# Kernel tuning notes

Hardware: AMD Instinct MI355X
Metric: run time of the kernel (lower is better)

The kernel has to match this reference:

```python
import jax, jax.numpy as jnp
import numpy as np

B, A, D, H = 32, 64, 128, 512
F = A * D  # 8192

def setup_inputs() -> dict:
    key = jax.random.key(0)
    ks = jax.random.split(key, 20)
    s = 0.02
    return {
        "swarm_states": jax.random.normal(ks[0], (B, A, D), jnp.float32),
        "swarm_goals": jax.random.normal(ks[1], (B, A, D), jnp.float32),
        # quantum layer stand-in: Linear(F->F) + tanh
        "Wq": jax.random.normal(ks[2], (F, F), jnp.float32) * s,
        "bq": jnp.zeros((F,), jnp.float32),
        # interaction_net: Linear(2D->H) ReLU Linear(H->H) ReLU Linear(H->D)
        "Wi1": jax.random.normal(ks[3], (2 * D, H), jnp.float32) * s,
        "bi1": jnp.zeros((H,), jnp.float32),
        "Wi2": jax.random.normal(ks[4], (H, H), jnp.float32) * s,
        "bi2": jnp.zeros((H,), jnp.float32),
        "Wi3": jax.random.normal(ks[5], (H, D), jnp.float32) * s,
        "bi3": jnp.zeros((D,), jnp.float32),
        # coordination_net: Linear(F->H) ReLU Linear(H->H) ReLU Linear(H->F)
        "Wc1": jax.random.normal(ks[6], (F, H), jnp.float32) * s,
        "bc1": jnp.zeros((H,), jnp.float32),
        "Wc2": jax.random.normal(ks[7], (H, H), jnp.float32) * s,
        "bc2": jnp.zeros((H,), jnp.float32),
        "Wc3": jax.random.normal(ks[8], (H, F), jnp.float32) * s,
        "bc3": jnp.zeros((F,), jnp.float32),
    }

def reference(swarm_states, swarm_goals, Wq, bq, Wi1, bi1, Wi2, bi2, Wi3, bi3,
              Wc1, bc1, Wc2, bc2, Wc3, bc3):
    b, a, d = swarm_states.shape
    states_flat = swarm_states.reshape(b, a * d)
    # quantum feature extraction (stand-in for QuantumNeuralLayer)
    quantum_features = jnp.tanh(states_flat @ Wq + bq)  # (B, A*D)

    # vectorized pairwise interaction MLP over all ordered (i, j) pairs
    xi = jnp.broadcast_to(swarm_states[:, :, None, :], (b, a, a, d))
    xj = jnp.broadcast_to(swarm_states[:, None, :, :], (b, a, a, d))
    pair = jnp.concatenate([xi, xj], axis=-1)            # (B, A, A, 2D)
    h = jax.nn.relu(pair @ Wi1 + bi1)
    h = jax.nn.relu(h @ Wi2 + bi2)
    inter = h @ Wi3 + bi3                                # (B, A, A, D)
    offdiag = (1.0 - jnp.eye(a, dtype=inter.dtype))[None, :, :, None]
    # per-agent aggregation over the other agents (mean over j != i)
    interactions = (inter * offdiag).sum(axis=2) / (a - 1)  # (B, A, D)

    c = jax.nn.relu(quantum_features @ Wc1 + bc1)
    c = jax.nn.relu(c @ Wc2 + bc2)
    coordination = (c @ Wc3 + bc3).reshape(b, a, d)      # (B, A, D)

    coordinated_states = swarm_states + 0.1 * interactions + 0.1 * coordination
    return coordinated_states, quantum_features, interactions, coordination
```

## Files before the change

kernel.cpp:

```cpp
#include <hip/hip_runtime.h>

typedef __attribute__((ext_vector_type(8))) short bf16x8;
typedef __attribute__((ext_vector_type(16))) float f32x16;
typedef _Float16 f16;
typedef __attribute__((ext_vector_type(8))) _Float16 f16x8;

static __device__ __forceinline__ unsigned short f2bf(float x) {
  unsigned int u = __float_as_uint(x);
  return (unsigned short)((u + 0x7FFFu + ((u >> 16) & 1u)) >> 16);
}
static __device__ __forceinline__ unsigned int pk2bf(float lo, float hi) {
  return ((unsigned int)f2bf(hi) << 16) | f2bf(lo);
}

static __device__ __forceinline__ f16x8 relu8(f16x8 x) {
  f16x8 z = {0, 0, 0, 0, 0, 0, 0, 0};
  return __builtin_elementwise_max(x, z);
}

__global__ __launch_bounds__(256) void tobf_kernel(const float* __restrict__ src,
                                                   unsigned short* __restrict__ dst) {
  const int idx = blockIdx.x * 256 + threadIdx.x;
  float4 v = ((const float4*)src)[idx];
  ushort4 o;
  o.x = f2bf(v.x); o.y = f2bf(v.y); o.z = f2bf(v.z); o.w = f2bf(v.w);
  ((ushort4*)dst)[idx] = o;
}

__global__ __launch_bounds__(256) void w2h_kernel(const float* __restrict__ Wi2,
                                                  f16* __restrict__ W2h) {
  __shared__ float tile[32][33];
  const int t = threadIdx.x;
  const int bk = blockIdx.x, bn = blockIdx.y;
  const int r = t >> 5, c = t & 31;
#pragma unroll
  for (int p = 0; p < 4; p++) {
    int rr = p * 8 + r;
    tile[rr][c] = Wi2[(bk * 32 + rr) * 512 + bn * 32 + c];
  }
  __syncthreads();
#pragma unroll
  for (int p = 0; p < 4; p++) {
    int rr = p * 8 + r;
    W2h[(bn * 32 + rr) * 512 + bk * 32 + c] = (f16)tile[c][rr];
  }
}

__global__ __launch_bounds__(256) void uvh_kernel(const float* __restrict__ S,
                                                  const float* __restrict__ Wi1,
                                                  const float* __restrict__ bi1,
                                                  f16* __restrict__ Uh, f16* __restrict__ Vh) {
  __shared__ float st[128][12];
  const int t = threadIdx.x;
  const int row0 = blockIdx.x * 8;
  for (int idx = t; idx < 1024; idx += 256) {
    int r = idx >> 7, k = idx & 127;
    st[k][r] = S[(row0 + r) * 128 + k];
  }
  __syncthreads();
  float au0[8], au1[8], av0[8], av1[8];
#pragma unroll
  for (int r = 0; r < 8; r++) { au0[r] = 0.f; au1[r] = 0.f; av0[r] = 0.f; av1[r] = 0.f; }
#pragma unroll 4
  for (int k = 0; k < 128; k++) {
    float wt0 = Wi1[k * 512 + t];
    float wt1 = Wi1[k * 512 + 256 + t];
    float wb0 = Wi1[(k + 128) * 512 + t];
    float wb1 = Wi1[(k + 128) * 512 + 256 + t];
    float4 sA = *(const float4*)&st[k][0];
    float4 sB = *(const float4*)&st[k][4];
    float s8[8] = {sA.x, sA.y, sA.z, sA.w, sB.x, sB.y, sB.z, sB.w};
#pragma unroll
    for (int r = 0; r < 8; r++) {
      au0[r] += s8[r] * wt0;
      au1[r] += s8[r] * wt1;
      av0[r] += s8[r] * wb0;
      av1[r] += s8[r] * wb1;
    }
  }
  const float b0 = bi1[t], b1 = bi1[256 + t];
#pragma unroll
  for (int r = 0; r < 8; r++) {
    Uh[(row0 + r) * 512 + t]       = (f16)(au0[r] + b0);
    Uh[(row0 + r) * 512 + 256 + t] = (f16)(au1[r] + b1);
    Vh[(row0 + r) * 512 + t]       = (f16)av0[r];
    Vh[(row0 + r) * 512 + 256 + t] = (f16)av1[r];
  }
}

__global__ __launch_bounds__(256, 4) void gemmw(const unsigned short* __restrict__ Abf,
                                                const float* __restrict__ W,
                                                float* __restrict__ P,
                                                int K, int N, int L, int l4sh) {
  __shared__ __align__(16) unsigned short As[32 * 512];
  const int t = threadIdx.x;
  const int k0 = blockIdx.y * L;
  const int L4 = L >> 2;
  const int swzm = 2 * L - 1;
  for (int idx = t; idx < (L << 3); idx += 256) {
    int row = idx >> l4sh, k4 = idx & (L4 - 1);
    ushort4 a4 = *(const ushort4*)&Abf[(size_t)row * K + k0 + k4 * 4];
    int off = (row * 2 * L + k4 * 8) ^ (((row & 7) << 4) & swzm);
    *(ushort4*)((char*)As + off) = a4;
  }
  __syncthreads();
  const int lane = t & 63, w = t >> 6;
  const int lrow = lane & 31, lh = lane >> 5;
  const int col = blockIdx.x * 128 + w * 32 + lrow;
  f32x16 acc0, acc1;
#pragma unroll
  for (int r = 0; r < 16; r++) { acc0[r] = 0.f; acc1[r] = 0.f; }
  const float* Wp = W + (size_t)(k0 + lh * 8) * N + col;
  const int aswz = ((lrow & 7) << 4) & swzm;
  const int abase = lrow * 2 * L + lh * 16;
  const int nks = L >> 4;
  int ks = 0;
  for (; ks + 1 < nks; ks += 2) {
    float wv0[8], wv1[8];
#pragma unroll
    for (int jj = 0; jj < 8; jj++) wv0[jj] = Wp[(size_t)(ks * 16 + jj) * N];
#pragma unroll
    for (int jj = 0; jj < 8; jj++) wv1[jj] = Wp[(size_t)(ks * 16 + 16 + jj) * N];
    uint4 b0, b1;
    b0.x = pk2bf(wv0[0], wv0[1]); b0.y = pk2bf(wv0[2], wv0[3]);
    b0.z = pk2bf(wv0[4], wv0[5]); b0.w = pk2bf(wv0[6], wv0[7]);
    b1.x = pk2bf(wv1[0], wv1[1]); b1.y = pk2bf(wv1[2], wv1[3]);
    b1.z = pk2bf(wv1[4], wv1[5]); b1.w = pk2bf(wv1[6], wv1[7]);
    bf16x8 af0 = *(const bf16x8*)((const char*)As + ((abase + ks * 32) ^ aswz));
    bf16x8 af1 = *(const bf16x8*)((const char*)As + ((abase + ks * 32 + 32) ^ aswz));
    acc0 = __builtin_amdgcn_mfma_f32_32x32x16_bf16(af0, *(const bf16x8*)&b0, acc0, 0, 0, 0);
    acc1 = __builtin_amdgcn_mfma_f32_32x32x16_bf16(af1, *(const bf16x8*)&b1, acc1, 0, 0, 0);
  }
  if (ks < nks) {
    float wv0[8];
#pragma unroll
    for (int jj = 0; jj < 8; jj++) wv0[jj] = Wp[(size_t)(ks * 16 + jj) * N];
    uint4 b0;
    b0.x = pk2bf(wv0[0], wv0[1]); b0.y = pk2bf(wv0[2], wv0[3]);
    b0.z = pk2bf(wv0[4], wv0[5]); b0.w = pk2bf(wv0[6], wv0[7]);
    bf16x8 af0 = *(const bf16x8*)((const char*)As + ((abase + ks * 32) ^ aswz));
    acc0 = __builtin_amdgcn_mfma_f32_32x32x16_bf16(af0, *(const bf16x8*)&b0, acc0, 0, 0, 0);
  }
  float* Pr = P + (size_t)blockIdx.y * 32 * N + col;
#pragma unroll
  for (int r = 0; r < 16; r++) {
    int row = (r & 3) + 8 * (r >> 2) + 4 * lh;
    Pr[(size_t)row * N] = acc0[r] + acc1[r];
  }
}

__global__ __launch_bounds__(256) void reduce_kernel(const float* __restrict__ P,
                                                     const float* __restrict__ bias,
                                                     float* __restrict__ dst,
                                                     unsigned short* __restrict__ dstbf,
                                                     int lnN, int KS, int act, int wbf) {
  const int idx = blockIdx.x * 256 + threadIdx.x;
  const int N = 1 << lnN;
  const int m = idx >> lnN, n = idx & (N - 1);
  float s = 0.f;
#pragma unroll 8
  for (int p = 0; p < KS; p++) s += P[((size_t)(p * 32 + m) << lnN) + n];
  s += bias[n];
  if (act == 1) s = fmaxf(s, 0.f);
  else if (act == 2) s = tanhf(s);
  dst[idx] = s;
  if (wbf) dstbf[idx] = f2bf(s);
}

__global__ __launch_bounds__(512, 2) void inter6_kernel(const f16* __restrict__ Uh,
                                                        const f16* __restrict__ Vh,
                                                        const f16* __restrict__ W2h,
                                                        const float* __restrict__ bi2,
                                                        float* __restrict__ Hsum) {
  __shared__ __align__(16) f16 Bt[128 * 512];
  __shared__ __align__(16) f16 Vc[64 * 128];
  const int t = threadIdx.x;
  const int nq = blockIdx.x;

#pragma unroll
  for (int i = 0; i < 16; i++) {
    int idx = i * 512 + t;
    int n = idx >> 6, ch = idx & 63;
    f16x8 w8 = *(const f16x8*)&W2h[(size_t)(nq * 128 + n) * 512 + ch * 8];
    int off = (n * 1024 + ch * 16) ^ ((n & 15) << 4);
    *(f16x8*)((char*)Bt + off) = w8;
  }

  const int w = t >> 6, lane = t & 63;
  const int ii = w & 1, tg = w >> 1;
  const int lrow = lane & 31, lh = lane >> 5;
  const char* Btc = (const char*)Bt;
  const char* Vcc = (const char*)Vc;
  char* Vcw = (char*)Vc;

  int bofs[4], bswz[4];
#pragma unroll
  for (int nf = 0; nf < 4; nf++) {
    int nr = nf * 32 + lrow;
    bofs[nf] = nr * 1024 + lh * 16;
    bswz[nf] = (nr & 15) << 4;
  }
  const int vofs0 = lrow * 256;
  const int vswz0 = (lrow & 15) << 4;
  const int vofs1 = (lrow + 32) * 256;
  const int vswz1 = vswz0;

  const int b = blockIdx.y >> 1;

  for (int s = 0; s < 4; s++) {
    const int tid = blockIdx.y * 16 + tg * 4 + s;
    const int it = tid & 31;
    const f16* Ub = Uh + (size_t)(b * 64 + it * 2 + ii) * 512 + lh * 8;

    f32x16 acc[2][4];
#pragma unroll
    for (int mf = 0; mf < 2; mf++)
#pragma unroll
      for (int nf = 0; nf < 4; nf++)
#pragma unroll
        for (int r = 0; r < 16; r++) acc[mf][nf][r] = 0.f;

    for (int ch = 0; ch < 4; ch++) {
      const int kc = ch * 128;
      __syncthreads();
#pragma unroll
      for (int i = 0; i < 2; i++) {
        int idx = i * 512 + t;
        int row = idx >> 4, c8 = idx & 15;
        f16x8 w8 = *(const f16x8*)&Vh[(size_t)(b * 64 + row) * 512 + kc + c8 * 8];
        *(f16x8*)(Vcw + ((row * 256 + c8 * 16) ^ ((row & 15) << 4))) = w8;
      }
      __syncthreads();
#pragma unroll
      for (int k16 = 0; k16 < 8; k16++) {
        const int kb2 = k16 * 32 + lh * 16;
        f16x8 v0 = *(const f16x8*)(Vcc + ((vofs0 + kb2) ^ vswz0));
        f16x8 v1 = *(const f16x8*)(Vcc + ((vofs1 + kb2) ^ vswz1));
        f16x8 u0 = *(const f16x8*)(Ub + kc + k16 * 16);
        f16x8 a0 = relu8(v0 + u0);
        f16x8 a1 = relu8(v1 + u0);
        const int kbyte = (kc + k16 * 16) * 2 + lh * 16 - lh * 16;
        (void)kbyte;
#pragma unroll
        for (int nf = 0; nf < 4; nf++) {
          f16x8 bfr = *(const f16x8*)(Btc + ((bofs[nf] + (kc + k16 * 16) * 2) ^ bswz[nf]));
          acc[0][nf] = __builtin_amdgcn_mfma_f32_32x32x16_f16(a0, bfr, acc[0][nf], 0, 0, 0);
          acc[1][nf] = __builtin_amdgcn_mfma_f32_32x32x16_f16(a1, bfr, acc[1][nf], 0, 0, 0);
        }
      }
    }

    const int iglob = it * 2 + ii;
    const int mf_d = iglob >> 5;
    const int rd = iglob & 31;
    const int lh_d = (rd >> 2) & 1;
    const int r_d = (rd & 3) + 4 * (rd >> 3);
#pragma unroll
    for (int nf = 0; nf < 4; nf++) {
      const int col = nq * 128 + nf * 32 + lrow;
      const float b2 = bi2[col];
      float ssum = 0.f;
#pragma unroll
      for (int mf = 0; mf < 2; mf++)
#pragma unroll
        for (int r = 0; r < 16; r++) {
          float x = fmaxf(acc[mf][nf][r] + b2, 0.f);
          if (mf == mf_d && r == r_d && lh == lh_d) x = 0.f;
          ssum += x;
        }
      ssum += __shfl_xor(ssum, 32);
      if (lh == 0) Hsum[(size_t)(b * 64 + iglob) * 512 + col] = ssum;
    }
  }
}

__global__ __launch_bounds__(256) void k3_kernel(const float* __restrict__ Hsum,
                                                 const float* __restrict__ Wi3,
                                                 const float* __restrict__ bi3,
                                                 float* __restrict__ inter) {
  __shared__ float st[512][10];
  const int t = threadIdx.x;
  const int row0 = blockIdx.x * 8;
  for (int idx = t; idx < 4096; idx += 256) {
    int r = idx >> 9, k = idx & 511;
    st[k][r] = Hsum[(row0 + r) * 512 + k] * (1.0f / 63.0f);
  }
  __syncthreads();
  const int c = t & 63;
  const int rg = t >> 6;
  float a0[2] = {0.f, 0.f}, a1[2] = {0.f, 0.f};
#pragma unroll 4
  for (int k = 0; k < 512; k++) {
    float w0 = Wi3[k * 128 + c];
    float w1 = Wi3[k * 128 + 64 + c];
    float2 h = *(const float2*)&st[k][rg * 2];
    a0[0] += h.x * w0; a0[1] += h.y * w0;
    a1[0] += h.x * w1; a1[1] += h.y * w1;
  }
  float b0 = bi3[c], b1 = bi3[64 + c];
#pragma unroll
  for (int r = 0; r < 2; r++) {
    inter[(row0 + rg * 2 + r) * 128 + c]      = a0[r] + b0;
    inter[(row0 + rg * 2 + r) * 128 + 64 + c] = a1[r] + b1;
  }
}

__global__ __launch_bounds__(256) void combine_kernel(const float* __restrict__ S,
                                                      const float* __restrict__ inter,
                                                      const float* __restrict__ coord,
                                                      float* __restrict__ out0) {
  const int i = blockIdx.x * 256 + threadIdx.x;
  float4 s = ((const float4*)S)[i];
  float4 a = ((const float4*)inter)[i];
  float4 c = ((const float4*)coord)[i];
  float4 o;
  o.x = s.x + 0.1f * (a.x + c.x);
  o.y = s.y + 0.1f * (a.y + c.y);
  o.z = s.z + 0.1f * (a.z + c.z);
  o.w = s.w + 0.1f * (a.w + c.w);
  ((float4*)out0)[i] = o;
}

extern "C" void kernel_launch(void* const* d_in, const int* in_sizes, int n_in,
                              void* d_out, int out_size, void* d_ws, size_t ws_size,
                              hipStream_t stream) {
  const float* states = (const float*)d_in[0];
  const float* Wq  = (const float*)d_in[2];
  const float* bq  = (const float*)d_in[3];
  const float* Wi1 = (const float*)d_in[4];
  const float* bi1 = (const float*)d_in[5];
  const float* Wi2 = (const float*)d_in[6];
  const float* bi2 = (const float*)d_in[7];
  const float* Wi3 = (const float*)d_in[8];
  const float* bi3 = (const float*)d_in[9];
  const float* Wc1 = (const float*)d_in[10];
  const float* bc1 = (const float*)d_in[11];
  const float* Wc2 = (const float*)d_in[12];
  const float* bc2 = (const float*)d_in[13];
  const float* Wc3 = (const float*)d_in[14];
  const float* bc3 = (const float*)d_in[15];

  float* out   = (float*)d_out;
  float* out0  = out;
  float* qf    = out + 262144;
  float* inter = out + 524288;
  float* coord = out + 786432;

  char* ws = (char*)d_ws;
  float*          P    = (float*)(ws);
  f16*            Uh   = (f16*)(ws + ((size_t)16 << 20));
  f16*            Vh   = (f16*)(ws + ((size_t)19 << 20));
  f16*            W2h  = (f16*)(ws + ((size_t)22 << 20));
  float*          Hsum = (float*)(ws + ((size_t)23 << 20));
  unsigned short* Sbf  = (unsigned short*)(ws + ((size_t)27 << 20));
  unsigned short* qfbf = (unsigned short*)(ws + ((size_t)28 << 20));
  float*          c1   = (float*)(ws + ((size_t)29 << 20));
  float*          c2   = (float*)(ws + ((size_t)29 << 20) + (1 << 16));
  unsigned short* c1bf = (unsigned short*)(ws + ((size_t)29 << 20) + (2 << 16));
  unsigned short* c2bf = (unsigned short*)(ws + ((size_t)29 << 20) + (3 << 16));

  tobf_kernel<<<256, 256, 0, stream>>>(states, Sbf);
  w2h_kernel<<<dim3(16, 16), 256, 0, stream>>>(Wi2, W2h);
  uvh_kernel<<<256, 256, 0, stream>>>(states, Wi1, bi1, Uh, Vh);

  gemmw<<<dim3(64, 16), 256, 0, stream>>>(Sbf, Wq, P, 8192, 8192, 512, 7);
  reduce_kernel<<<1024, 256, 0, stream>>>(P, bq, qf, qfbf, 13, 16, 2, 1);

  inter6_kernel<<<dim3(4, 64), 512, 0, stream>>>(Uh, Vh, W2h, bi2, Hsum);
  k3_kernel<<<256, 256, 0, stream>>>(Hsum, Wi3, bi3, inter);

  gemmw<<<dim3(4, 64), 256, 0, stream>>>(qfbf, Wc1, P, 8192, 512, 128, 5);
  reduce_kernel<<<64, 256, 0, stream>>>(P, bc1, c1, c1bf, 9, 64, 1, 1);
  gemmw<<<dim3(4, 32), 256, 0, stream>>>(c1bf, Wc2, P, 512, 512, 16, 2);
  reduce_kernel<<<64, 256, 0, stream>>>(P, bc2, c2, c2bf, 9, 32, 1, 1);
  gemmw<<<dim3(64, 8), 256, 0, stream>>>(c2bf, Wc3, P, 512, 8192, 64, 4);
  reduce_kernel<<<1024, 256, 0, stream>>>(P, bc3, coord, qfbf, 13, 8, 0, 0);

  combine_kernel<<<256, 256, 0, stream>>>(states, inter, coord, out0);
}
```

Before: 225.6 us.

## Merge prep and tail kernels, co-schedule k3 with Wc1 GEMM, prefetch weights

Three prep kernels are merged into one block-indexed prep kernel. The k3 projection and the Wc1 split-K GEMM are fused into one launch so their blocks run concurrently. The final combine is folded into the last reduce. The gemmw inner loop now software-prefetches four weight fragments ahead of the MFMAs, clamped at the K edge, to hide global-load latency. This cuts launch count and exposes overlap, at the cost of more registers and a larger shared allocation for the fused kernel.

```diff
diff --git a/kernel.cpp b/kernel.cpp
--- a/kernel.cpp
+++ b/kernel.cpp
@@ -12,89 +12,101 @@
 static __device__ __forceinline__ unsigned int pk2bf(float lo, float hi) {
   return ((unsigned int)f2bf(hi) << 16) | f2bf(lo);
 }
-
 static __device__ __forceinline__ f16x8 relu8(f16x8 x) {
   f16x8 z = {0, 0, 0, 0, 0, 0, 0, 0};
   return __builtin_elementwise_max(x, z);
 }
 
-__global__ __launch_bounds__(256) void tobf_kernel(const float* __restrict__ src,
-                                                   unsigned short* __restrict__ dst) {
-  const int idx = blockIdx.x * 256 + threadIdx.x;
-  float4 v = ((const float4*)src)[idx];
-  ushort4 o;
-  o.x = f2bf(v.x); o.y = f2bf(v.y); o.z = f2bf(v.z); o.w = f2bf(v.w);
-  ((ushort4*)dst)[idx] = o;
-}
-
-__global__ __launch_bounds__(256) void w2h_kernel(const float* __restrict__ Wi2,
-                                                  f16* __restrict__ W2h) {
-  __shared__ float tile[32][33];
+__global__ __launch_bounds__(256) void prep_kernel(const float* __restrict__ states,
+                                                   const float* __restrict__ Wi2,
+                                                   const float* __restrict__ Wi1,
+                                                   const float* __restrict__ bi1,
+                                                   unsigned short* __restrict__ Sbf,
+                                                   f16* __restrict__ W2h,
+                                                   f16* __restrict__ Uh, f16* __restrict__ Vh) {
+  __shared__ float lds_f[1536];
   const int t = threadIdx.x;
-  const int bk = blockIdx.x, bn = blockIdx.y;
-  const int r = t >> 5, c = t & 31;
-#pragma unroll
-  for (int p = 0; p < 4; p++) {
-    int rr = p * 8 + r;
-    tile[rr][c] = Wi2[(bk * 32 + rr) * 512 + bn * 32 + c];
-  }
-  __syncthreads();
-#pragma unroll
-  for (int p = 0; p < 4; p++) {
-    int rr = p * 8 + r;
-    W2h[(bn * 32 + rr) * 512 + bk * 32 + c] = (f16)tile[c][rr];
-  }
-}
-
-__global__ __launch_bounds__(256) void uvh_kernel(const float* __restrict__ S,
-                                                  const float* __restrict__ Wi1,
-                                                  const float* __restrict__ bi1,
-                                                  f16* __restrict__ Uh, f16* __restrict__ Vh) {
-  __shared__ float st[128][12];
-  const int t = threadIdx.x;
-  const int row0 = blockIdx.x * 8;
-  for (int idx = t; idx < 1024; idx += 256) {
-    int r = idx >> 7, k = idx & 127;
-    st[k][r] = S[(row0 + r) * 128 + k];
-  }
-  __syncthreads();
-  float au0[8], au1[8], av0[8], av1[8];
-#pragma unroll
-  for (int r = 0; r < 8; r++) { au0[r] = 0.f; au1[r] = 0.f; av0[r] = 0.f; av1[r] = 0.f; }
+  const int bid = blockIdx.x;
+  if (bid < 256) {
+    const int idx = bid * 256 + t;
+    float4 v = ((const float4*)states)[idx];
+    ushort4 o;
+    o.x = f2bf(v.x); o.y = f2bf(v.y); o.z = f2bf(v.z); o.w = f2bf(v.w);
+    ((ushort4*)Sbf)[idx] = o;
+  } else if (bid < 512) {
+    const int b = bid - 256;
+    const int bk = b & 15, bn = b >> 4;
+    float (*tile)[33] = (float(*)[33])lds_f;
+    const int r = t >> 5, c = t & 31;
+#pragma unroll
+    for (int p = 0; p < 4; p++) {
+      int rr = p * 8 + r;
+      tile[rr][c] = Wi2[(bk * 32 + rr) * 512 + bn * 32 + c];
+    }
+    __syncthreads();
+#pragma unroll
+    for (int p = 0; p < 4; p++) {
+      int rr = p * 8 + r;
+      W2h[(bn * 32 + rr) * 512 + bk * 32 + c] = (f16)tile[c][rr];
+    }
+  } else {
+    const int row0 = (bid - 512) * 8;
+    float (*st)[12] = (float(*)[12])lds_f;
+    for (int idx = t; idx < 1024; idx += 256) {
+      int r = idx >> 7, k = idx & 127;
+      st[k][r] = states[(row0 + r) * 128 + k];
+    }
+    __syncthreads();
+    float au0[8], au1[8], av0[8], av1[8];
+#pragma unroll
+    for (int r = 0; r < 8; r++) { au0[r] = 0.f; au1[r] = 0.f; av0[r] = 0.f; av1[r] = 0.f; }
 #pragma unroll 4
-  for (int k = 0; k < 128; k++) {
-    float wt0 = Wi1[k * 512 + t];
-    float wt1 = Wi1[k * 512 + 256 + t];
-    float wb0 = Wi1[(k + 128) * 512 + t];
-    float wb1 = Wi1[(k + 128) * 512 + 256 + t];
-    float4 sA = *(const float4*)&st[k][0];
-    float4 sB = *(const float4*)&st[k][4];
-    float s8[8] = {sA.x, sA.y, sA.z, sA.w, sB.x, sB.y, sB.z, sB.w};
+    for (int k = 0; k < 128; k++) {
+      float wt0 = Wi1[k * 512 + t];
+      float wt1 = Wi1[k * 512 + 256 + t];
+      float wb0 = Wi1[(k + 128) * 512 + t];
+      float wb1 = Wi1[(k + 128) * 512 + 256 + t];
+      float4 sA = *(const float4*)&st[k][0];
+      float4 sB = *(const float4*)&st[k][4];
+      float s8[8] = {sA.x, sA.y, sA.z, sA.w, sB.x, sB.y, sB.z, sB.w};
+#pragma unroll
+      for (int r = 0; r < 8; r++) {
+        au0[r] += s8[r] * wt0;
+        au1[r] += s8[r] * wt1;
+        av0[r] += s8[r] * wb0;
+        av1[r] += s8[r] * wb1;
+      }
+    }
+    const float b0 = bi1[t], b1 = bi1[256 + t];
 #pragma unroll
     for (int r = 0; r < 8; r++) {
-      au0[r] += s8[r] * wt0;
-      au1[r] += s8[r] * wt1;
-      av0[r] += s8[r] * wb0;
-      av1[r] += s8[r] * wb1;
-    }
-  }
-  const float b0 = bi1[t], b1 = bi1[256 + t];
-#pragma unroll
-  for (int r = 0; r < 8; r++) {
-    Uh[(row0 + r) * 512 + t]       = (f16)(au0[r] + b0);
-    Uh[(row0 + r) * 512 + 256 + t] = (f16)(au1[r] + b1);
-    Vh[(row0 + r) * 512 + t]       = (f16)av0[r];
-    Vh[(row0 + r) * 512 + 256 + t] = (f16)av1[r];
-  }
-}
-
-__global__ __launch_bounds__(256, 4) void gemmw(const unsigned short* __restrict__ Abf,
-                                                const float* __restrict__ W,
-                                                float* __restrict__ P,
-                                                int K, int N, int L, int l4sh) {
-  __shared__ __align__(16) unsigned short As[32 * 512];
-  const int t = threadIdx.x;
-  const int k0 = blockIdx.y * L;
+      Uh[(row0 + r) * 512 + t]       = (f16)(au0[r] + b0);
+      Uh[(row0 + r) * 512 + 256 + t] = (f16)(au1[r] + b1);
+      Vh[(row0 + r) * 512 + t]       = (f16)av0[r];
+      Vh[(row0 + r) * 512 + 256 + t] = (f16)av1[r];
+    }
+  }
+}
+
+static __device__ __forceinline__ void gw_load(const float* __restrict__ Wp, int N, int ksrow,
+                                               float w[8]) {
+#pragma unroll
+  for (int jj = 0; jj < 8; jj++) w[jj] = Wp[(size_t)(ksrow + jj) * N];
+}
+static __device__ __forceinline__ bf16x8 gw_pack(const float w[8]) {
+  uint4 b;
+  b.x = pk2bf(w[0], w[1]); b.y = pk2bf(w[2], w[3]);
+  b.z = pk2bf(w[4], w[5]); b.w = pk2bf(w[6], w[7]);
+  return *(const bf16x8*)&b;
+}
+
+static __device__ __forceinline__ void gemmw_body(unsigned short* As ,
+                                                  const unsigned short* __restrict__ Abf,
+                                                  const float* __restrict__ W,
+                                                  float* __restrict__ P,
+                                                  int K, int N, int L, int l4sh,
+                                                  int t, int nb, int ksl) {
+  const int k0 = ksl * L;
   const int L4 = L >> 2;
   const int swzm = 2 * L - 1;
   for (int idx = t; idx < (L << 3); idx += 256) {
@@ -106,54 +118,69 @@
   __syncthreads();
   const int lane = t & 63, w = t >> 6;
   const int lrow = lane & 31, lh = lane >> 5;
-  const int col = blockIdx.x * 128 + w * 32 + lrow;
-  f32x16 acc0, acc1;
-#pragma unroll
-  for (int r = 0; r < 16; r++) { acc0[r] = 0.f; acc1[r] = 0.f; }
+  const int col = nb * 128 + w * 32 + lrow;
   const float* Wp = W + (size_t)(k0 + lh * 8) * N + col;
   const int aswz = ((lrow & 7) << 4) & swzm;
   const int abase = lrow * 2 * L + lh * 16;
   const int nks = L >> 4;
+  const int rmax = K - (k0 + lh * 8) - 8;
+
+  f32x16 acc0, acc1;
+#pragma unroll
+  for (int r = 0; r < 16; r++) { acc0[r] = 0.f; acc1[r] = 0.f; }
+
+  float w0[8], w1[8], w2[8], w3[8];
+  gw_load(Wp, N, 0, w0);
+  gw_load(Wp, N, min(16, rmax), w1);
+  gw_load(Wp, N, min(32, rmax), w2);
+  gw_load(Wp, N, min(48, rmax), w3);
+
   int ks = 0;
-  for (; ks + 1 < nks; ks += 2) {
-    float wv0[8], wv1[8];
-#pragma unroll
-    for (int jj = 0; jj < 8; jj++) wv0[jj] = Wp[(size_t)(ks * 16 + jj) * N];
-#pragma unroll
-    for (int jj = 0; jj < 8; jj++) wv1[jj] = Wp[(size_t)(ks * 16 + 16 + jj) * N];
-    uint4 b0, b1;
-    b0.x = pk2bf(wv0[0], wv0[1]); b0.y = pk2bf(wv0[2], wv0[3]);
-    b0.z = pk2bf(wv0[4], wv0[5]); b0.w = pk2bf(wv0[6], wv0[7]);
-    b1.x = pk2bf(wv1[0], wv1[1]); b1.y = pk2bf(wv1[2], wv1[3]);
-    b1.z = pk2bf(wv1[4], wv1[5]); b1.w = pk2bf(wv1[6], wv1[7]);
+  for (; ks + 3 < nks; ks += 4) {
     bf16x8 af0 = *(const bf16x8*)((const char*)As + ((abase + ks * 32) ^ aswz));
     bf16x8 af1 = *(const bf16x8*)((const char*)As + ((abase + ks * 32 + 32) ^ aswz));
-    acc0 = __builtin_amdgcn_mfma_f32_32x32x16_bf16(af0, *(const bf16x8*)&b0, acc0, 0, 0, 0);
-    acc1 = __builtin_amdgcn_mfma_f32_32x32x16_bf16(af1, *(const bf16x8*)&b1, acc1, 0, 0, 0);
-  }
-  if (ks < nks) {
-    float wv0[8];
-#pragma unroll
-    for (int jj = 0; jj < 8; jj++) wv0[jj] = Wp[(size_t)(ks * 16 + jj) * N];
-    uint4 b0;
-    b0.x = pk2bf(wv0[0], wv0[1]); b0.y = pk2bf(wv0[2], wv0[3]);
-    b0.z = pk2bf(wv0[4], wv0[5]); b0.w = pk2bf(wv0[6], wv0[7]);
-    bf16x8 af0 = *(const bf16x8*)((const char*)As + ((abase + ks * 32) ^ aswz));
-    acc0 = __builtin_amdgcn_mfma_f32_32x32x16_bf16(af0, *(const bf16x8*)&b0, acc0, 0, 0, 0);
-  }
-  float* Pr = P + (size_t)blockIdx.y * 32 * N + col;
+    bf16x8 af2 = *(const bf16x8*)((const char*)As + ((abase + ks * 32 + 64) ^ aswz));
+    bf16x8 af3 = *(const bf16x8*)((const char*)As + ((abase + ks * 32 + 96) ^ aswz));
+    acc0 = __builtin_amdgcn_mfma_f32_32x32x16_bf16(af0, gw_pack(w0), acc0, 0, 0, 0);
+    gw_load(Wp, N, min((ks + 4) * 16, rmax), w0);
+    acc1 = __builtin_amdgcn_mfma_f32_32x32x16_bf16(af1, gw_pack(w1), acc1, 0, 0, 0);
+    gw_load(Wp, N, min((ks + 5) * 16, rmax), w1);
+    acc0 = __builtin_amdgcn_mfma_f32_32x32x16_bf16(af2, gw_pack(w2), acc0, 0, 0, 0);
+    gw_load(Wp, N, min((ks + 6) * 16, rmax), w2);
+    acc1 = __builtin_amdgcn_mfma_f32_32x32x16_bf16(af3, gw_pack(w3), acc1, 0, 0, 0);
+    gw_load(Wp, N, min((ks + 7) * 16, rmax), w3);
+  }
+  for (; ks < nks; ks++) {
+    float wt[8];
+    gw_load(Wp, N, ks * 16, wt);
+    bf16x8 af = *(const bf16x8*)((const char*)As + ((abase + ks * 32) ^ aswz));
+    acc0 = __builtin_amdgcn_mfma_f32_32x32x16_bf16(af, gw_pack(wt), acc0, 0, 0, 0);
+  }
+
+  float* Pr = P + (size_t)ksl * 32 * N + col;
 #pragma unroll
   for (int r = 0; r < 16; r++) {
     int row = (r & 3) + 8 * (r >> 2) + 4 * lh;
     Pr[(size_t)row * N] = acc0[r] + acc1[r];
   }
+}
+
+__global__ __launch_bounds__(256, 4) void gemmw(const unsigned short* __restrict__ Abf,
+                                                const float* __restrict__ W,
+                                                float* __restrict__ P,
+                                                int K, int N, int L, int l4sh) {
+  __shared__ __align__(16) unsigned short As[32 * 512];
+  gemmw_body(As, Abf, W, P, K, N, L, l4sh, threadIdx.x, blockIdx.x, blockIdx.y);
 }
 
 __global__ __launch_bounds__(256) void reduce_kernel(const float* __restrict__ P,
                                                      const float* __restrict__ bias,
                                                      float* __restrict__ dst,
                                                      unsigned short* __restrict__ dstbf,
-                                                     int lnN, int KS, int act, int wbf) {
+                                                     int lnN, int KS, int act, int wbf,
+                                                     const float* __restrict__ S,
+                                                     const float* __restrict__ Ip,
+                                                     float* __restrict__ out0, int comb) {
   const int idx = blockIdx.x * 256 + threadIdx.x;
   const int N = 1 << lnN;
   const int m = idx >> lnN, n = idx & (N - 1);
@@ -165,6 +192,7 @@
   else if (act == 2) s = tanhf(s);
   dst[idx] = s;
   if (wbf) dstbf[idx] = f2bf(s);
+  if (comb) out0[idx] = S[idx] + 0.1f * (Ip[idx] + s);
 }
 
 __global__ __launch_bounds__(512, 2) void inter6_kernel(const f16* __restrict__ Uh,
@@ -239,8 +267,6 @@
         f16x8 u0 = *(const f16x8*)(Ub + kc + k16 * 16);
         f16x8 a0 = relu8(v0 + u0);
         f16x8 a1 = relu8(v1 + u0);
-        const int kbyte = (kc + k16 * 16) * 2 + lh * 16 - lh * 16;
-        (void)kbyte;
 #pragma unroll
         for (int nf = 0; nf < 4; nf++) {
           f16x8 bfr = *(const f16x8*)(Btc + ((bofs[nf] + (kc + k16 * 16) * 2) ^ bswz[nf]));
@@ -274,13 +300,12 @@
   }
 }
 
-__global__ __launch_bounds__(256) void k3_kernel(const float* __restrict__ Hsum,
-                                                 const float* __restrict__ Wi3,
-                                                 const float* __restrict__ bi3,
-                                                 float* __restrict__ inter) {
-  __shared__ float st[512][10];
-  const int t = threadIdx.x;
-  const int row0 = blockIdx.x * 8;
+static __device__ __forceinline__ void k3_body(float (*st)[10],
+                                               const float* __restrict__ Hsum,
+                                               const float* __restrict__ Wi3,
+                                               const float* __restrict__ bi3,
+                                               float* __restrict__ inter, int t, int blk) {
+  const int row0 = blk * 8;
   for (int idx = t; idx < 4096; idx += 256) {
     int r = idx >> 9, k = idx & 511;
     st[k][r] = Hsum[(row0 + r) * 512 + k] * (1.0f / 63.0f);
@@ -305,20 +330,22 @@
   }
 }
 
-__global__ __launch_bounds__(256) void combine_kernel(const float* __restrict__ S,
-                                                      const float* __restrict__ inter,
-                                                      const float* __restrict__ coord,
-                                                      float* __restrict__ out0) {
-  const int i = blockIdx.x * 256 + threadIdx.x;
-  float4 s = ((const float4*)S)[i];
-  float4 a = ((const float4*)inter)[i];
-  float4 c = ((const float4*)coord)[i];
-  float4 o;
-  o.x = s.x + 0.1f * (a.x + c.x);
-  o.y = s.y + 0.1f * (a.y + c.y);
-  o.z = s.z + 0.1f * (a.z + c.z);
-  o.w = s.w + 0.1f * (a.w + c.w);
-  ((float4*)out0)[i] = o;
+__global__ __launch_bounds__(256, 4) void k3c1_kernel(const float* __restrict__ Hsum,
+                                                      const float* __restrict__ Wi3,
+                                                      const float* __restrict__ bi3,
+                                                      float* __restrict__ inter,
+                                                      const unsigned short* __restrict__ qfbf,
+                                                      const float* __restrict__ Wc1,
+                                                      float* __restrict__ P) {
+  __shared__ __align__(16) char lds[32768];
+  const int t = threadIdx.x;
+  const int bid = blockIdx.x;
+  if (bid < 256) {
+    k3_body((float(*)[10])lds, Hsum, Wi3, bi3, inter, t, bid);
+  } else {
+    const int b = bid - 256;
+    gemmw_body((unsigned short*)lds, qfbf, Wc1, P, 8192, 512, 128, 5, t, b & 3, b >> 2);
+  }
 }
 
 extern "C" void kernel_launch(void* const* d_in, const int* in_sizes, int n_in,
@@ -359,22 +386,23 @@
   unsigned short* c1bf = (unsigned short*)(ws + ((size_t)29 << 20) + (2 << 16));
   unsigned short* c2bf = (unsigned short*)(ws + ((size_t)29 << 20) + (3 << 16));
 
-  tobf_kernel<<<256, 256, 0, stream>>>(states, Sbf);
-  w2h_kernel<<<dim3(16, 16), 256, 0, stream>>>(Wi2, W2h);
-  uvh_kernel<<<256, 256, 0, stream>>>(states, Wi1, bi1, Uh, Vh);
+  prep_kernel<<<768, 256, 0, stream>>>(states, Wi2, Wi1, bi1, Sbf, W2h, Uh, Vh);
 
   gemmw<<<dim3(64, 16), 256, 0, stream>>>(Sbf, Wq, P, 8192, 8192, 512, 7);
-  reduce_kernel<<<1024, 256, 0, stream>>>(P, bq, qf, qfbf, 13, 16, 2, 1);
+  reduce_kernel<<<1024, 256, 0, stream>>>(P, bq, qf, qfbf, 13, 16, 2, 1,
+                                          nullptr, nullptr, nullptr, 0);
 
   inter6_kernel<<<dim3(4, 64), 512, 0, stream>>>(Uh, Vh, W2h, bi2, Hsum);
-  k3_kernel<<<256, 256, 0, stream>>>(Hsum, Wi3, bi3, inter);
-
-  gemmw<<<dim3(4, 64), 256, 0, stream>>>(qfbf, Wc1, P, 8192, 512, 128, 5);
-  reduce_kernel<<<64, 256, 0, stream>>>(P, bc1, c1, c1bf, 9, 64, 1, 1);
+
+  k3c1_kernel<<<512, 256, 0, stream>>>(Hsum, Wi3, bi3, inter, qfbf, Wc1, P);
+  reduce_kernel<<<64, 256, 0, stream>>>(P, bc1, c1, c1bf, 9, 64, 1, 1,
+                                        nullptr, nullptr, nullptr, 0);
+
   gemmw<<<dim3(4, 32), 256, 0, stream>>>(c1bf, Wc2, P, 512, 512, 16, 2);
-  reduce_kernel<<<64, 256, 0, stream>>>(P, bc2, c2, c2bf, 9, 32, 1, 1);
+  reduce_kernel<<<64, 256, 0, stream>>>(P, bc2, c2, c2bf, 9, 32, 1, 1,
+                                        nullptr, nullptr, nullptr, 0);
+
   gemmw<<<dim3(64, 8), 256, 0, stream>>>(c2bf, Wc3, P, 512, 8192, 64, 4);
-  reduce_kernel<<<1024, 256, 0, stream>>>(P, bc3, coord, qfbf, 13, 8, 0, 0);
-
-  combine_kernel<<<256, 256, 0, stream>>>(states, inter, coord, out0);
-}
+  reduce_kernel<<<1024, 256, 0, stream>>>(P, bc3, coord, nullptr, 13, 8, 0, 0,
+                                          states, inter, out0, 1);
+}
```

New measurement: 237.2 us. 1.05x slower.
